# Optimization experiments

Measured on AMD Instinct MI355X. Metric: run time of the kernel, lower is better.

The kernel has to match this reference:

```python
import jax, jax.numpy as jnp
import numpy as np

B, S, D, H = 2, 2048, 2048, 16
HD = D // H  # head_dim = 128


def setup_inputs() -> dict:
    key = jax.random.key(0)
    k1, k2, k3, k4, k5, k6 = jax.random.split(key, 6)
    scale = 1.0 / np.sqrt(D)
    return {
        "hidden_states": jax.random.normal(k1, (B, S, D), dtype=jnp.float32),
        "attention_mask": jnp.ones((B, S), dtype=jnp.int32),
        "wq": jax.random.normal(k2, (D, D), dtype=jnp.float32) * scale,
        "wk": jax.random.normal(k3, (D, D), dtype=jnp.float32) * scale,
        "wv": jax.random.normal(k4, (D, D), dtype=jnp.float32) * scale,
        "wo": jax.random.normal(k5, (D, D), dtype=jnp.float32) * scale,
        "bo": jax.random.normal(k6, (D,), dtype=jnp.float32) * 0.01,
    }


def reference(hidden_states, attention_mask, wq, wk, wv, wo, bo):
    b, s, d = hidden_states.shape
    # QKV projections (no bias), split heads -> [B, S, H, HD]
    q = (hidden_states @ wq).reshape(b, s, H, HD)
    k = (hidden_states @ wk).reshape(b, s, H, HD)
    v = (hidden_states @ wv).reshape(b, s, H, HD)

    # combined causal + padding mask -> [B, 1, S, S]
    causal = jnp.tril(jnp.ones((s, s), dtype=bool))[None, None]
    pad = (attention_mask > 0)[:, None, None, :]  # [B,1,1,S]
    mask = jnp.logical_and(causal, pad)

    big_neg = jnp.finfo(hidden_states.dtype).min
    bias = jnp.where(mask, 0.0, big_neg).astype(hidden_states.dtype)

    # scaled dot-product attention (flax dot_product_attention scales by 1/sqrt(head_dim))
    scores = jnp.einsum("bqhd,bkhd->bhqk", q, k) / jnp.sqrt(jnp.asarray(HD, hidden_states.dtype))
    probs = jax.nn.softmax(scores + bias, axis=-1)
    ctx = jnp.einsum("bhqk,bkhd->bqhd", probs, v).reshape(b, s, d)

    return ctx @ wo + bo
```

## Files before the change

### kernel.cpp

```cpp
#include <hip/hip_runtime.h>
#include <hip/hip_bf16.h>
#include <stdint.h>

#define Bv 2
#define Sv 2048
#define Dv 2048
#define Hv 16
#define HDv 128
#define Mv (Bv*Sv)

typedef __attribute__((ext_vector_type(8))) short short8;
typedef __attribute__((ext_vector_type(4))) short short4v;
typedef __attribute__((ext_vector_type(4))) float f32x4;

__device__ __forceinline__ unsigned short bf16_rne(float f) {
    union { float f; uint32_t u; } c; c.f = f;
    uint32_t u = c.u;
    u += 0x7fffu + ((u >> 16) & 1u);
    return (unsigned short)(u >> 16);
}

__device__ __forceinline__ uint32_t cvt_pk_bf16(float lo, float hi) {
    uint32_t r;
    asm("v_cvt_pk_bf16_f32 %0, %1, %2" : "=v"(r) : "v"(lo), "v"(hi));
    return r;
}

__device__ __forceinline__ void gload16(const void* g, void* l) {
    __builtin_amdgcn_global_load_lds((const __attribute__((address_space(1))) void*)g,
                                     (__attribute__((address_space(3))) void*)l, 16, 0, 0);
}

#define BARRIER() asm volatile("s_barrier" ::: "memory")
#define LGKM0()   do { asm volatile("s_waitcnt lgkmcnt(0)" ::: "memory"); \
                       __builtin_amdgcn_sched_barrier(0); } while (0)

__global__ void cvt_x_kernel(const float* __restrict__ x, unsigned short* __restrict__ xb) {
    int i = (blockIdx.x * 256 + threadIdx.x) * 4;
    float4 v = *(const float4*)(x + i);
    short4v o;
    o[0] = (short)bf16_rne(v.x);
    o[1] = (short)bf16_rne(v.y);
    o[2] = (short)bf16_rne(v.z);
    o[3] = (short)bf16_rne(v.w);
    *(short4v*)(xb + i) = o;
}

__global__ void cvt_wt_kernel(const float* __restrict__ w0, const float* __restrict__ w1,
                              const float* __restrict__ w2, const float* __restrict__ w3,
                              unsigned short* __restrict__ wt) {
    __shared__ unsigned short t[64][65];
    int z = blockIdx.z;
    const float* w = (z == 0) ? w0 : (z == 1) ? w1 : (z == 2) ? w2 : w3;
    unsigned short* o = wt + (size_t)z * Dv * Dv;
    int k0 = blockIdx.x * 64, n0 = blockIdx.y * 64;
    for (int i = threadIdx.x; i < 4096; i += 256) {
        int r = i >> 6, c = i & 63;
        t[r][c] = bf16_rne(w[(size_t)(k0 + r) * Dv + n0 + c]);
    }
    __syncthreads();
    for (int i = threadIdx.x; i < 4096; i += 256) {
        int r = i >> 6, c = i & 63;
        o[(size_t)(n0 + r) * Dv + k0 + c] = t[c][r];
    }
}

__global__ void vt_kernel(const unsigned short* __restrict__ V, unsigned short* __restrict__ VT) {
    __shared__ unsigned short t[64 * 64];
    const int tid = threadIdx.x;
    const int b = blockIdx.z;
    const int s0 = blockIdx.x * 64, c0 = blockIdx.y * 64;
    const unsigned short* Vb = V + (size_t)b * Sv * Dv;
    unsigned short* VTb = VT + (size_t)b * Dv * Sv;
    #pragma unroll
    for (int ii = 0; ii < 2; ++ii) {
        int i = tid + ii * 256;
        int r = i >> 3, ch = i & 7;
        short8 v = *(const short8*)&Vb[(size_t)(s0 + r) * Dv + c0 + ch * 8];
        *(short8*)&t[r * 64 + ((ch ^ (r & 7)) << 3)] = v;
    }
    __syncthreads();
    #pragma unroll
    for (int ii = 0; ii < 2; ++ii) {
        int o = tid + ii * 256;
        int orow = o >> 3, och = o & 7;
        short8 v;
        #pragma unroll
        for (int j = 0; j < 8; ++j) {
            int r = och * 8 + j;
            int c = orow;
            v[j] = (short)t[r * 64 + ((((c >> 3) ^ (r & 7)) << 3) | (c & 7))];
        }
        *(short8*)&VTb[(size_t)(c0 + orow) * Sv + s0 + och * 8] = v;
    }
}

__global__ __launch_bounds__(512, 2) void gemm8ph_kernel(
    const unsigned short* __restrict__ A,
    const unsigned short* __restrict__ WtBase,
    unsigned short* __restrict__ CbBase)
{
    extern __shared__ unsigned short lds[];
    const int tid = threadIdx.x;
    const int wv = tid >> 6, ln = tid & 63;
    const int lr = ln & 15, lg = ln >> 4;
    const int wm = wv >> 2, wn = wv & 3;

    const int bid = blockIdx.x;
    const int xcd = bid & 7, idx = bid >> 3;
    const int n_idx = xcd * 2 + idx / 16;
    const int m_idx = idx % 16;
    const int m0 = m_idx * 256, n0g = n_idx * 256;

    const int lrow = wv * 8 + (ln >> 3);
    const int lcol = ((ln & 7) ^ (ln >> 3)) << 3;
    const unsigned short* Ag = A      + (size_t)(m0  + lrow) * Dv + lcol;
    const unsigned short* Bg = WtBase + (size_t)(n0g + lrow) * Dv + lcol;

    auto SH = [&](int T, int isB, int h) {
        const unsigned short* src = (isB ? Bg : Ag) + (size_t)(h * 128) * Dv + T * 64;
        unsigned short* dst = &lds[(T & 1) * 32768 + isB * 16384 + h * 8192 + wv * 512];
        gload16(src, dst);
        gload16(src + (size_t)64 * Dv, dst + 4096);
    };

    const int axk = lr & 7;
    auto RDA = [&](int buf, int fm, int ks) {
        return *(const short8*)&lds[buf * 32768 + (wm * 128 + fm * 16 + lr) * 64 + (((ks * 4 + lg) ^ axk) << 3)];
    };
    auto RDB = [&](int buf, int fn, int ks) {
        return *(const short8*)&lds[buf * 32768 + 16384 + (wn * 64 + fn * 16 + lr) * 64 + (((ks * 4 + lg) ^ axk) << 3)];
    };

    f32x4 acc[8][4];
    #pragma unroll
    for (int fm = 0; fm < 8; fm++)
        #pragma unroll
        for (int fn = 0; fn < 4; fn++)
            acc[fm][fn] = (f32x4){0.f, 0.f, 0.f, 0.f};

    SH(0, 0, 0); SH(0, 0, 1); SH(0, 1, 0); SH(0, 1, 1);
    SH(1, 1, 0); SH(1, 0, 0);
    asm volatile("s_waitcnt vmcnt(4)" ::: "memory");
    BARRIER();

    short8 af[8], b0[4], b1[4];
    const int NT2 = 16;

    #define MFMA_BLK(FN0, FN1, BARR) do {                                              \
        __builtin_amdgcn_s_setprio(1);                                                 \
        _Pragma("unroll")                                                              \
        for (int fm = 0; fm < 8; fm++) {                                               \
            acc[fm][FN0] = __builtin_amdgcn_mfma_f32_16x16x32_bf16(af[fm], BARR[FN0], acc[fm][FN0], 0, 0, 0); \
            acc[fm][FN1] = __builtin_amdgcn_mfma_f32_16x16x32_bf16(af[fm], BARR[FN1], acc[fm][FN1], 0, 0, 0); \
        }                                                                              \
        __builtin_amdgcn_s_setprio(0);                                                 \
    } while (0)

    for (int i = 0; i < NT2; ++i) {
        const int Tb = 2 * i + 1;
        const bool more = (i + 1 < NT2);

        #pragma unroll
        for (int fm = 0; fm < 8; fm++) af[fm] = RDA(0, fm, 0);
        #pragma unroll
        for (int fn = 0; fn < 4; fn++) b0[fn] = RDB(0, fn, 0);
        SH(Tb, 0, 1);
        BARRIER(); LGKM0();
        MFMA_BLK(0, 1, b0);
        BARRIER();

        #pragma unroll
        for (int fn = 0; fn < 4; fn++) b1[fn] = RDB(0, fn, 1);
        SH(Tb, 1, 1);
        BARRIER(); LGKM0();
        MFMA_BLK(2, 3, b0);
        BARRIER();

        #pragma unroll
        for (int fm = 0; fm < 8; fm++) af[fm] = RDA(0, fm, 1);
        if (more) SH(Tb + 1, 1, 0);
        BARRIER(); LGKM0();
        MFMA_BLK(0, 1, b1);
        BARRIER();

        if (more) SH(Tb + 1, 0, 0);
        BARRIER(); LGKM0();
        MFMA_BLK(2, 3, b1);
        if (more) asm volatile("s_waitcnt vmcnt(4)" ::: "memory");
        else      asm volatile("s_waitcnt vmcnt(0)" ::: "memory");
        BARRIER();

        #pragma unroll
        for (int fm = 0; fm < 8; fm++) af[fm] = RDA(1, fm, 0);
        #pragma unroll
        for (int fn = 0; fn < 4; fn++) b0[fn] = RDB(1, fn, 0);
        if (more) SH(Tb + 1, 0, 1);
        BARRIER(); LGKM0();
        MFMA_BLK(0, 1, b0);
        BARRIER();

        #pragma unroll
        for (int fn = 0; fn < 4; fn++) b1[fn] = RDB(1, fn, 1);
        if (more) SH(Tb + 1, 1, 1);
        BARRIER(); LGKM0();
        MFMA_BLK(2, 3, b0);
        BARRIER();

        #pragma unroll
        for (int fm = 0; fm < 8; fm++) af[fm] = RDA(1, fm, 1);
        if (more) SH(Tb + 2, 1, 0);
        BARRIER(); LGKM0();
        MFMA_BLK(0, 1, b1);
        BARRIER();

        if (more) SH(Tb + 2, 0, 0);
        BARRIER(); LGKM0();
        MFMA_BLK(2, 3, b1);
        if (more) {
            asm volatile("s_waitcnt vmcnt(4)" ::: "memory");
            BARRIER();
        }
    }
    #undef MFMA_BLK

    const int z = n0g >> 11;
    unsigned short* Cz = CbBase + (size_t)z * Mv * Dv;
    const int ncl = (n0g & 2047) + wn * 64;
    #pragma unroll
    for (int fm = 0; fm < 8; fm++)
        #pragma unroll
        for (int fn = 0; fn < 4; fn++) {
            int row = m0 + wm * 128 + fm * 16 + lg * 4;
            int col = ncl + fn * 16 + lr;
            #pragma unroll
            for (int r = 0; r < 4; r++)
                Cz[(size_t)(row + r) * Dv + col] = bf16_rne(acc[fm][fn][r]);
        }
}

template<int FOUT>
__global__ __launch_bounds__(512, 2) void gemm8_kernel(
    const unsigned short* __restrict__ A,
    const unsigned short* __restrict__ WtBase,
    unsigned short* __restrict__ Cb,
    float* __restrict__ Cf,
    const float* __restrict__ bias)
{
    extern __shared__ unsigned short lds[];
    const int tid = threadIdx.x;
    const int wv = tid >> 6, ln = tid & 63;
    const int lr = ln & 15, lg = ln >> 4;
    const int wm = wv >> 2, wn = wv & 3;

    const int bid = blockIdx.x;
    const int xcd = bid & 7, idx = bid >> 3;
    const int n_idx = xcd;
    const int m_idx = idx;
    const int m0 = m_idx * 128;
    const int n0g = n_idx * 256;
    const int NT = Dv / 64;

    const int srow = ln >> 3;
    const int swz = ((ln & 7) ^ srow) << 3;
    const unsigned short* Ab = A      + (size_t)(m0  + wv * 8 + srow) * Dv + swz;
    const unsigned short* Bb = WtBase + (size_t)(n0g + wv * 8 + srow) * Dv + swz;

    auto STAGE_A = [&](int t, int d) {
        const unsigned short* g = Ab + t * 64;
        #pragma unroll
        for (int j = 0; j < 2; ++j)
            gload16(g + (size_t)(j * 64) * Dv, &lds[d * 24576 + (j * 64 + wv * 8) * 64]);
    };
    auto STAGE_B = [&](int t, int d) {
        const unsigned short* g = Bb + t * 64;
        #pragma unroll
        for (int j = 0; j < 4; ++j)
            gload16(g + (size_t)(j * 64) * Dv, &lds[d * 24576 + 8192 + (j * 64 + wv * 8) * 64]);
    };

    const int aro = (wm * 64 + lr) * 64;
    const int bro = (wn * 64 + lr) * 64;
    const int ach0 = ((lg ^ (lr & 7)) << 3);
    const int ach1 = (((4 + lg) ^ (lr & 7)) << 3);

    f32x4 acc[4][4];
    #pragma unroll
    for (int mi = 0; mi < 4; mi++)
        #pragma unroll
        for (int ni = 0; ni < 4; ni++)
            acc[mi][ni] = (f32x4){0.f, 0.f, 0.f, 0.f};

    STAGE_A(0, 0); STAGE_B(0, 0);
    STAGE_A(1, 1); STAGE_B(1, 1);
    asm volatile("s_waitcnt vmcnt(6)" ::: "memory");
    BARRIER();

    for (int t = 0; t < NT; ++t) {
        const int d = t % 3, d2 = (t + 2) % 3;
        const unsigned short* la = &lds[d * 24576];
        const unsigned short* lb = &lds[d * 24576 + 8192];

        short8 af[4][2], bf0[2][2];
        #pragma unroll
        for (int mi = 0; mi < 4; mi++) {
            af[mi][0] = *(const short8*)&la[aro + mi * 1024 + ach0];
            af[mi][1] = *(const short8*)&la[aro + mi * 1024 + ach1];
        }
        #pragma unroll
        for (int ni = 0; ni < 2; ni++) {
            bf0[ni][0] = *(const short8*)&lb[bro + ni * 1024 + ach0];
            bf0[ni][1] = *(const short8*)&lb[bro + ni * 1024 + ach1];
        }
        if (t + 2 < NT) STAGE_A(t + 2, d2);
        BARRIER();
        __builtin_amdgcn_s_setprio(1);
        #pragma unroll
        for (int mi = 0; mi < 4; mi++)
            #pragma unroll
            for (int ni = 0; ni < 2; ni++) {
                acc[mi][ni] = __builtin_amdgcn_mfma_f32_16x16x32_bf16(af[mi][0], bf0[ni][0], acc[mi][ni], 0, 0, 0);
                acc[mi][ni] = __builtin_amdgcn_mfma_f32_16x16x32_bf16(af[mi][1], bf0[ni][1], acc[mi][ni], 0, 0, 0);
            }
        __builtin_amdgcn_s_setprio(0);

        short8 bf1[2][2];
        #pragma unroll
        for (int ni = 0; ni < 2; ni++) {
            bf1[ni][0] = *(const short8*)&lb[bro + (ni + 2) * 1024 + ach0];
            bf1[ni][1] = *(const short8*)&lb[bro + (ni + 2) * 1024 + ach1];
        }
        if (t + 2 < NT) STAGE_B(t + 2, d2);
        asm volatile("s_waitcnt vmcnt(6)" ::: "memory");
        BARRIER();
        __builtin_amdgcn_s_setprio(1);
        #pragma unroll
        for (int mi = 0; mi < 4; mi++)
            #pragma unroll
            for (int ni = 0; ni < 2; ni++) {
                acc[mi][ni + 2] = __builtin_amdgcn_mfma_f32_16x16x32_bf16(af[mi][0], bf1[ni][0], acc[mi][ni + 2], 0, 0, 0);
                acc[mi][ni + 2] = __builtin_amdgcn_mfma_f32_16x16x32_bf16(af[mi][1], bf1[ni][1], acc[mi][ni + 2], 0, 0, 0);
            }
        __builtin_amdgcn_s_setprio(0);
    }

    #pragma unroll
    for (int mi = 0; mi < 4; mi++)
        #pragma unroll
        for (int ni = 0; ni < 4; ni++) {
            int row = m0 + wm * 64 + mi * 16 + lg * 4;
            int col = n0g + wn * 64 + ni * 16 + lr;
            if (FOUT) {
                float bv = bias[col];
                #pragma unroll
                for (int r = 0; r < 4; r++)
                    Cf[(size_t)(row + r) * Dv + col] = acc[mi][ni][r] + bv;
            } else {
                #pragma unroll
                for (int r = 0; r < 4; r++)
                    Cb[(size_t)(row + r) * Dv + col] = bf16_rne(acc[mi][ni][r]);
            }
        }
}

__global__ __launch_bounds__(512) void attn_kernel(
    const unsigned short* __restrict__ Q, const unsigned short* __restrict__ K,
    const unsigned short* __restrict__ VT, const int* __restrict__ pmask,
    unsigned short* __restrict__ CTX)
{
    __shared__ unsigned short lK[2][64 * 128];
    __shared__ unsigned short lVt[2][128 * 64];
    __shared__ int lPmB[2][64];
    __shared__ int lPmOk[2];

    const int tid = threadIdx.x, wv = tid >> 6, ln = tid & 63;
    const int lr = ln & 15, lg = ln >> 4;
    const int L = blockIdx.x;
    const int bh = (L & 7) * 4 + ((L >> 3) & 3);
    const int b = bh >> 4, h = bh & 15;
    const int v = L >> 5;
    const int qidx = (v < 8) ? (15 - v) : (v - 8);
    const int q0 = qidx * 128;
    const int qw0 = q0 + wv * 16;
    const size_t hoff  = (size_t)b * Sv * Dv + (size_t)h * HDv;
    const size_t vtoff = ((size_t)b * Dv + (size_t)h * HDv) * Sv;

    short8 qf[4];
    #pragma unroll
    for (int ds = 0; ds < 4; ds++)
        qf[ds] = *(const short8*)&Q[hoff + (size_t)(qw0 + lr) * Dv + ds * 32 + lg * 8];

    size_t koff[2], voff[2];
    #pragma unroll
    for (int ii = 0; ii < 2; ++ii) {
        int slot = ii * 512 + wv * 64 + ln;
        int krow = slot >> 4, kch = slot & 15;
        koff[ii] = hoff + (size_t)krow * Dv + ((kch ^ (krow & 7)) << 3);
        int vrow = slot >> 3, vch = slot & 7;
        voff[ii] = vtoff + (size_t)vrow * Sv + ((vch ^ (vrow & 7)) << 3);
    }

    auto STAGE = [&](int t, int buf) {
        const size_t kadd = (size_t)(t << 6) * Dv;
        const int vadd = t << 6;
        unsigned short* kb = &lK[buf][0];
        unsigned short* vb = &lVt[buf][0];
        #pragma unroll
        for (int ii = 0; ii < 2; ++ii) {
            gload16(K + koff[ii] + kadd, kb + (ii * 512 + wv * 64) * 8);
            gload16(VT + voff[ii] + vadd, vb + (ii * 512 + wv * 64) * 8);
        }
        if (wv == 0) {
            int pmv = pmask[b * Sv + (t << 6) + ln];
            lPmB[buf][ln] = pmv;
            unsigned long long bal = __ballot(pmv != 0);
            if (ln == 0) lPmOk[buf] = (bal == ~0ull) ? 1 : 0;
        }
    };

    f32x4 acc[8];
    #pragma unroll
    for (int n = 0; n < 8; n++) acc[n] = (f32x4){0.f, 0.f, 0.f, 0.f};
    float mrow = -3.0e38f, lrow = 0.f;
    const float CS = 0.12751744f;
    const int qg = qw0 + lr;
    const int nt = (q0 >> 6) + 2;
    const int srcA = lr + ((lg & 1) << 5);
    const int srcB = srcA + 16;
    const bool hiSel = (lg >= 2);

    auto TILE = [&](int t, int buf, auto CAUSAL_c) {
        constexpr bool CAUSAL = decltype(CAUSAL_c)::value;
        const int kv0 = t << 6;
        const unsigned short* kb = &lK[buf][0];
        const unsigned short* vb = &lVt[buf][0];

        f32x4 st[4];
        #pragma unroll
        for (int t2 = 0; t2 < 4; ++t2) st[t2] = (f32x4){0.f, 0.f, 0.f, 0.f};
        __builtin_amdgcn_s_setprio(1);
        #pragma unroll
        for (int t2 = 0; t2 < 4; ++t2) {
            const int krow = t2 * 16 + lr;
            #pragma unroll
            for (int ds = 0; ds < 4; ++ds) {
                const int ch = ds * 4 + lg;
                short8 kf = *(const short8*)&kb[krow * 128 + ((ch ^ (krow & 7)) << 3)];
                st[t2] = __builtin_amdgcn_mfma_f32_16x16x32_bf16(kf, qf[ds], st[t2], 0, 0, 0);
            }
        }
        __builtin_amdgcn_s_setprio(0);

        float sv[4][4];
        float rmax;
        if constexpr (CAUSAL) {
            const int* pm = &lPmB[buf][0];
            #pragma unroll
            for (int t2 = 0; t2 < 4; ++t2)
                #pragma unroll
                for (int r = 0; r < 4; ++r) {
                    int kvl = t2 * 16 + lg * 4 + r;
                    bool ok = ((kv0 + kvl) <= qg) && (pm[kvl] != 0);
                    sv[t2][r] = ok ? st[t2][r] * CS : -1.0e30f;
                }
            rmax = sv[0][0];
            #pragma unroll
            for (int t2 = 0; t2 < 4; ++t2)
                #pragma unroll
                for (int r = 0; r < 4; ++r) rmax = fmaxf(rmax, sv[t2][r]);
            rmax = fmaxf(rmax, __shfl_xor(rmax, 16, 64));
            rmax = fmaxf(rmax, __shfl_xor(rmax, 32, 64));
        } else {
            rmax = st[0][0];
            #pragma unroll
            for (int t2 = 0; t2 < 4; ++t2)
                #pragma unroll
                for (int r = 0; r < 4; ++r) rmax = fmaxf(rmax, st[t2][r]);
            rmax = fmaxf(rmax, __shfl_xor(rmax, 16, 64));
            rmax = fmaxf(rmax, __shfl_xor(rmax, 32, 64));
            rmax *= CS;
        }

        if (!__all(rmax - mrow <= 8.0f)) {
            float mn = fmaxf(mrow, rmax);
            float alpha = exp2f(mrow - mn);
            mrow = mn;
            lrow *= alpha;
            #pragma unroll
            for (int n = 0; n < 8; n++)
                #pragma unroll
                for (int r = 0; r < 4; r++) acc[n][r] *= alpha;
        }

        float p[4][4]; float psum = 0.f;
        if constexpr (CAUSAL) {
            #pragma unroll
            for (int t2 = 0; t2 < 4; ++t2)
                #pragma unroll
                for (int r = 0; r < 4; ++r) {
                    float e = exp2f(sv[t2][r] - mrow);
                    p[t2][r] = (sv[t2][r] > -5.0e29f) ? e : 0.f;
                    psum += p[t2][r];
                }
        } else {
            if (lPmOk[buf]) {
                #pragma unroll
                for (int t2 = 0; t2 < 4; ++t2)
                    #pragma unroll
                    for (int r = 0; r < 4; ++r) {
                        p[t2][r] = exp2f(fmaf(st[t2][r], CS, -mrow));
                        psum += p[t2][r];
                    }
            } else {
                const int* pm = &lPmB[buf][0];
                #pragma unroll
                for (int t2 = 0; t2 < 4; ++t2)
                    #pragma unroll
                    for (int r = 0; r < 4; ++r) {
                        int kvl = t2 * 16 + lg * 4 + r;
                        float e = exp2f(fmaf(st[t2][r], CS, -mrow));
                        p[t2][r] = (pm[kvl] != 0) ? e : 0.f;
                        psum += p[t2][r];
                    }
            }
        }
        psum += __shfl_xor(psum, 16, 64);
        psum += __shfl_xor(psum, 32, 64);
        lrow += psum;

        uint32_t pk[4][2];
        #pragma unroll
        for (int t2 = 0; t2 < 4; ++t2)
            #pragma unroll
            for (int pp = 0; pp < 2; ++pp)
                pk[t2][pp] = cvt_pk_bf16(p[t2][2 * pp], p[t2][2 * pp + 1]);

        union U { uint32_t u[4]; short8 s; } pa0, pa1;
        {
            uint32_t l0 = (uint32_t)__shfl((int)pk[0][0], srcA, 64), h0 = (uint32_t)__shfl((int)pk[1][0], srcA, 64);
            uint32_t l1 = (uint32_t)__shfl((int)pk[0][1], srcA, 64), h1 = (uint32_t)__shfl((int)pk[1][1], srcA, 64);
            uint32_t l2 = (uint32_t)__shfl((int)pk[0][0], srcB, 64), h2 = (uint32_t)__shfl((int)pk[1][0], srcB, 64);
            uint32_t l3 = (uint32_t)__shfl((int)pk[0][1], srcB, 64), h3 = (uint32_t)__shfl((int)pk[1][1], srcB, 64);
            pa0.u[0] = hiSel ? h0 : l0; pa0.u[1] = hiSel ? h1 : l1;
            pa0.u[2] = hiSel ? h2 : l2; pa0.u[3] = hiSel ? h3 : l3;
        }
        {
            uint32_t l0 = (uint32_t)__shfl((int)pk[2][0], srcA, 64), h0 = (uint32_t)__shfl((int)pk[3][0], srcA, 64);
            uint32_t l1 = (uint32_t)__shfl((int)pk[2][1], srcA, 64), h1 = (uint32_t)__shfl((int)pk[3][1], srcA, 64);
            uint32_t l2 = (uint32_t)__shfl((int)pk[2][0], srcB, 64), h2 = (uint32_t)__shfl((int)pk[3][0], srcB, 64);
            uint32_t l3 = (uint32_t)__shfl((int)pk[2][1], srcB, 64), h3 = (uint32_t)__shfl((int)pk[3][1], srcB, 64);
            pa1.u[0] = hiSel ? h0 : l0; pa1.u[1] = hiSel ? h1 : l1;
            pa1.u[2] = hiSel ? h2 : l2; pa1.u[3] = hiSel ? h3 : l3;
        }

        __builtin_amdgcn_s_setprio(1);
        #pragma unroll
        for (int n = 0; n < 8; n++) {
            const int vrow = n * 16 + lr;
            short8 a0 = *(const short8*)&vb[vrow * 64 + ((lg ^ (vrow & 7)) << 3)];
            acc[n] = __builtin_amdgcn_mfma_f32_16x16x32_bf16(a0, pa0.s, acc[n], 0, 0, 0);
            short8 a1 = *(const short8*)&vb[vrow * 64 + (((4 + lg) ^ (vrow & 7)) << 3)];
            acc[n] = __builtin_amdgcn_mfma_f32_16x16x32_bf16(a1, pa1.s, acc[n], 0, 0, 0);
        }
        __builtin_amdgcn_s_setprio(0);
    };

    STAGE(0, 0);
    __syncthreads();
    int cur = 0;

    for (int t = 0; t < nt; ++t) {
        if (t + 1 < nt) STAGE(t + 1, cur ^ 1);
        const int kv0 = t << 6;
        if (kv0 <= qw0 + 15) {
            if (kv0 + 63 > qw0) TILE(t, cur, std::integral_constant<bool, true>{});
            else                TILE(t, cur, std::integral_constant<bool, false>{});
        }
        __syncthreads();
        cur ^= 1;
    }

    float inv = 1.0f / lrow;
    #pragma unroll
    for (int n = 0; n < 8; n++) {
        short4v o;
        #pragma unroll
        for (int r = 0; r < 4; r++) o[r] = (short)bf16_rne(acc[n][r] * inv);
        *(short4v*)&CTX[hoff + (size_t)qg * Dv + n * 16 + lg * 4] = o;
    }
}

extern "C" void kernel_launch(void* const* d_in, const int* in_sizes, int n_in,
                              void* d_out, int out_size, void* d_ws, size_t ws_size,
                              hipStream_t stream) {
    const float* hs  = (const float*)d_in[0];
    const int*   am  = (const int*)d_in[1];
    const float* wq  = (const float*)d_in[2];
    const float* wk  = (const float*)d_in[3];
    const float* wv_ = (const float*)d_in[4];
    const float* wo  = (const float*)d_in[5];
    const float* bo  = (const float*)d_in[6];
    float* out = (float*)d_out;

    char* ws = (char*)d_ws;
    unsigned short* Xb  = (unsigned short*)ws;
    unsigned short* Wt  = (unsigned short*)(ws + (size_t)16 * 1024 * 1024);
    unsigned short* QKV = (unsigned short*)(ws + (size_t)48 * 1024 * 1024);
    unsigned short* CTX = (unsigned short*)(ws + (size_t)96 * 1024 * 1024);
    unsigned short* VT  = Xb;

    const int LDSB_8PH = 131072;
    const int LDSB_R   = 147456;
    static bool attrSet = false;
    if (!attrSet) {
        hipFuncSetAttribute((const void*)gemm8ph_kernel, hipFuncAttributeMaxDynamicSharedMemorySize, LDSB_8PH);
        hipFuncSetAttribute((const void*)gemm8_kernel<0>, hipFuncAttributeMaxDynamicSharedMemorySize, LDSB_R);
        hipFuncSetAttribute((const void*)gemm8_kernel<1>, hipFuncAttributeMaxDynamicSharedMemorySize, LDSB_R);
        attrSet = true;
    }

    hipLaunchKernelGGL(cvt_x_kernel, dim3(Mv * Dv / 4 / 256), dim3(256), 0, stream, hs, Xb);
    hipLaunchKernelGGL(cvt_wt_kernel, dim3(32, 32, 4), dim3(256), 0, stream, wq, wk, wv_, wo, Wt);
    hipLaunchKernelGGL(gemm8ph_kernel, dim3(256), dim3(512), LDSB_8PH, stream, Xb, Wt, QKV);
    hipLaunchKernelGGL(gemm8_kernel<0>, dim3(256), dim3(512), LDSB_R, stream,
                       Xb, Wt + 2 * (size_t)Dv * Dv, QKV + 2 * (size_t)Mv * Dv, (float*)nullptr, (const float*)nullptr);
    hipLaunchKernelGGL(vt_kernel, dim3(32, 32, 2), dim3(256), 0, stream,
                       QKV + 2 * (size_t)Mv * Dv, VT);
    hipLaunchKernelGGL(attn_kernel, dim3(512), dim3(512), 0, stream,
                       QKV, QKV + (size_t)Mv * Dv, VT, am, CTX);
    hipLaunchKernelGGL(gemm8_kernel<1>, dim3(256), dim3(512), LDSB_R, stream,
                       CTX, Wt + 3 * (size_t)Dv * Dv, (unsigned short*)nullptr, out, bo);
}
```

Baseline: 237.7 us.

## Pair low and high causal query tiles per block to share K/V tiles

Each attention block now handles two 128-row query tiles, a low one and its mirror high one, with separate accumulators and softmax state. Each staged K/V tile feeds both groups, so LDS K/V fragments are reused and the causal work per block is balanced. The grid drops from 512 to 256 blocks. The cost is roughly doubled accumulator registers, which may lower occupancy, plus fewer blocks to spread across the CUs.

```diff
diff --git a/kernel.cpp b/kernel.cpp
--- a/kernel.cpp
+++ b/kernel.cpp
@@ -12,6 +12,8 @@
 typedef __attribute__((ext_vector_type(8))) short short8;
 typedef __attribute__((ext_vector_type(4))) short short4v;
 typedef __attribute__((ext_vector_type(4))) float f32x4;
+
+union PU { uint32_t u[4]; short8 s; };
 
 __device__ __forceinline__ unsigned short bf16_rne(float f) {
     union { float f; uint32_t u; } c; c.f = f;
@@ -378,17 +380,18 @@
     const int L = blockIdx.x;
     const int bh = (L & 7) * 4 + ((L >> 3) & 3);
     const int b = bh >> 4, h = bh & 15;
-    const int v = L >> 5;
-    const int qidx = (v < 8) ? (15 - v) : (v - 8);
-    const int q0 = qidx * 128;
-    const int qw0 = q0 + wv * 16;
+    const int p = L >> 5;
+    const int q0l = p * 128, q0h = (15 - p) * 128;
+    const int qw0l = q0l + wv * 16, qw0h = q0h + wv * 16;
     const size_t hoff  = (size_t)b * Sv * Dv + (size_t)h * HDv;
     const size_t vtoff = ((size_t)b * Dv + (size_t)h * HDv) * Sv;
 
-    short8 qf[4];
-    #pragma unroll
-    for (int ds = 0; ds < 4; ds++)
-        qf[ds] = *(const short8*)&Q[hoff + (size_t)(qw0 + lr) * Dv + ds * 32 + lg * 8];
+    short8 qfL[4], qfH[4];
+    #pragma unroll
+    for (int ds = 0; ds < 4; ds++) {
+        qfL[ds] = *(const short8*)&Q[hoff + (size_t)(qw0l + lr) * Dv + ds * 32 + lg * 8];
+        qfH[ds] = *(const short8*)&Q[hoff + (size_t)(qw0h + lr) * Dv + ds * 32 + lg * 8];
+    }
 
     size_t koff[2], voff[2];
     #pragma unroll
@@ -418,42 +421,27 @@
         }
     };
 
-    f32x4 acc[8];
-    #pragma unroll
-    for (int n = 0; n < 8; n++) acc[n] = (f32x4){0.f, 0.f, 0.f, 0.f};
-    float mrow = -3.0e38f, lrow = 0.f;
+    f32x4 accL[8], accH[8];
+    #pragma unroll
+    for (int n = 0; n < 8; n++) {
+        accL[n] = (f32x4){0.f, 0.f, 0.f, 0.f};
+        accH[n] = (f32x4){0.f, 0.f, 0.f, 0.f};
+    }
+    float mrowL = -3.0e38f, lrowL = 0.f;
+    float mrowH = -3.0e38f, lrowH = 0.f;
     const float CS = 0.12751744f;
-    const int qg = qw0 + lr;
-    const int nt = (q0 >> 6) + 2;
+    const int qgL = qw0l + lr, qgH = qw0h + lr;
+    const int nt = (q0h >> 6) + 2;
     const int srcA = lr + ((lg & 1) << 5);
     const int srcB = srcA + 16;
     const bool hiSel = (lg >= 2);
 
-    auto TILE = [&](int t, int buf, auto CAUSAL_c) {
-        constexpr bool CAUSAL = decltype(CAUSAL_c)::value;
-        const int kv0 = t << 6;
-        const unsigned short* kb = &lK[buf][0];
-        const unsigned short* vb = &lVt[buf][0];
-
-        f32x4 st[4];
-        #pragma unroll
-        for (int t2 = 0; t2 < 4; ++t2) st[t2] = (f32x4){0.f, 0.f, 0.f, 0.f};
-        __builtin_amdgcn_s_setprio(1);
-        #pragma unroll
-        for (int t2 = 0; t2 < 4; ++t2) {
-            const int krow = t2 * 16 + lr;
-            #pragma unroll
-            for (int ds = 0; ds < 4; ++ds) {
-                const int ch = ds * 4 + lg;
-                short8 kf = *(const short8*)&kb[krow * 128 + ((ch ^ (krow & 7)) << 3)];
-                st[t2] = __builtin_amdgcn_mfma_f32_16x16x32_bf16(kf, qf[ds], st[t2], 0, 0, 0);
-            }
-        }
-        __builtin_amdgcn_s_setprio(0);
-
+    auto GROUP_SM = [&](const f32x4 (&st)[4], f32x4 (&acc)[8], float& mrow, float& lrow,
+                        int qg, int kv0, int buf, PU& pa0, PU& pa1, auto DIAG_c) {
+        constexpr bool DIAG = decltype(DIAG_c)::value;
         float sv[4][4];
         float rmax;
-        if constexpr (CAUSAL) {
+        if constexpr (DIAG) {
             const int* pm = &lPmB[buf][0];
             #pragma unroll
             for (int t2 = 0; t2 < 4; ++t2)
@@ -492,15 +480,15 @@
                 for (int r = 0; r < 4; r++) acc[n][r] *= alpha;
         }
 
-        float p[4][4]; float psum = 0.f;
-        if constexpr (CAUSAL) {
+        float pr[4][4]; float psum = 0.f;
+        if constexpr (DIAG) {
             #pragma unroll
             for (int t2 = 0; t2 < 4; ++t2)
                 #pragma unroll
                 for (int r = 0; r < 4; ++r) {
                     float e = exp2f(sv[t2][r] - mrow);
-                    p[t2][r] = (sv[t2][r] > -5.0e29f) ? e : 0.f;
-                    psum += p[t2][r];
+                    pr[t2][r] = (sv[t2][r] > -5.0e29f) ? e : 0.f;
+                    psum += pr[t2][r];
                 }
         } else {
             if (lPmOk[buf]) {
@@ -508,8 +496,8 @@
                 for (int t2 = 0; t2 < 4; ++t2)
                     #pragma unroll
                     for (int r = 0; r < 4; ++r) {
-                        p[t2][r] = exp2f(fmaf(st[t2][r], CS, -mrow));
-                        psum += p[t2][r];
+                        pr[t2][r] = exp2f(fmaf(st[t2][r], CS, -mrow));
+                        psum += pr[t2][r];
                     }
             } else {
                 const int* pm = &lPmB[buf][0];
@@ -519,8 +507,8 @@
                     for (int r = 0; r < 4; ++r) {
                         int kvl = t2 * 16 + lg * 4 + r;
                         float e = exp2f(fmaf(st[t2][r], CS, -mrow));
-                        p[t2][r] = (pm[kvl] != 0) ? e : 0.f;
-                        psum += p[t2][r];
+                        pr[t2][r] = (pm[kvl] != 0) ? e : 0.f;
+                        psum += pr[t2][r];
                     }
             }
         }
@@ -533,9 +521,8 @@
         for (int t2 = 0; t2 < 4; ++t2)
             #pragma unroll
             for (int pp = 0; pp < 2; ++pp)
-                pk[t2][pp] = cvt_pk_bf16(p[t2][2 * pp], p[t2][2 * pp + 1]);
-
-        union U { uint32_t u[4]; short8 s; } pa0, pa1;
+                pk[t2][pp] = cvt_pk_bf16(pr[t2][2 * pp], pr[t2][2 * pp + 1]);
+
         {
             uint32_t l0 = (uint32_t)__shfl((int)pk[0][0], srcA, 64), h0 = (uint32_t)__shfl((int)pk[1][0], srcA, 64);
             uint32_t l1 = (uint32_t)__shfl((int)pk[0][1], srcA, 64), h1 = (uint32_t)__shfl((int)pk[1][1], srcA, 64);
@@ -552,15 +539,52 @@
             pa1.u[0] = hiSel ? h0 : l0; pa1.u[1] = hiSel ? h1 : l1;
             pa1.u[2] = hiSel ? h2 : l2; pa1.u[3] = hiSel ? h3 : l3;
         }
+    };
+
+    auto TILE = [&](int t, int buf, auto DOL_c, auto DIAG_c) {
+        constexpr bool DOL = decltype(DOL_c)::value;
+        const int kv0 = t << 6;
+        const unsigned short* kb = &lK[buf][0];
+        const unsigned short* vb = &lVt[buf][0];
+
+        f32x4 stL[4], stH[4];
+        #pragma unroll
+        for (int t2 = 0; t2 < 4; ++t2) {
+            stH[t2] = (f32x4){0.f, 0.f, 0.f, 0.f};
+            if constexpr (DOL) stL[t2] = (f32x4){0.f, 0.f, 0.f, 0.f};
+        }
+        __builtin_amdgcn_s_setprio(1);
+        #pragma unroll
+        for (int t2 = 0; t2 < 4; ++t2) {
+            const int krow = t2 * 16 + lr;
+            #pragma unroll
+            for (int ds = 0; ds < 4; ++ds) {
+                const int ch = ds * 4 + lg;
+                short8 kf = *(const short8*)&kb[krow * 128 + ((ch ^ (krow & 7)) << 3)];
+                stH[t2] = __builtin_amdgcn_mfma_f32_16x16x32_bf16(kf, qfH[ds], stH[t2], 0, 0, 0);
+                if constexpr (DOL)
+                    stL[t2] = __builtin_amdgcn_mfma_f32_16x16x32_bf16(kf, qfL[ds], stL[t2], 0, 0, 0);
+            }
+        }
+        __builtin_amdgcn_s_setprio(0);
+
+        PU paH0, paH1, paL0, paL1;
+        GROUP_SM(stH, accH, mrowH, lrowH, qgH, kv0, buf, paH0, paH1, DIAG_c);
+        if constexpr (DOL)
+            GROUP_SM(stL, accL, mrowL, lrowL, qgL, kv0, buf, paL0, paL1, DIAG_c);
 
         __builtin_amdgcn_s_setprio(1);
         #pragma unroll
         for (int n = 0; n < 8; n++) {
             const int vrow = n * 16 + lr;
             short8 a0 = *(const short8*)&vb[vrow * 64 + ((lg ^ (vrow & 7)) << 3)];
-            acc[n] = __builtin_amdgcn_mfma_f32_16x16x32_bf16(a0, pa0.s, acc[n], 0, 0, 0);
             short8 a1 = *(const short8*)&vb[vrow * 64 + (((4 + lg) ^ (vrow & 7)) << 3)];
-            acc[n] = __builtin_amdgcn_mfma_f32_16x16x32_bf16(a1, pa1.s, acc[n], 0, 0, 0);
+            accH[n] = __builtin_amdgcn_mfma_f32_16x16x32_bf16(a0, paH0.s, accH[n], 0, 0, 0);
+            accH[n] = __builtin_amdgcn_mfma_f32_16x16x32_bf16(a1, paH1.s, accH[n], 0, 0, 0);
+            if constexpr (DOL) {
+                accL[n] = __builtin_amdgcn_mfma_f32_16x16x32_bf16(a0, paL0.s, accL[n], 0, 0, 0);
+                accL[n] = __builtin_amdgcn_mfma_f32_16x16x32_bf16(a1, paL1.s, accL[n], 0, 0, 0);
+            }
         }
         __builtin_amdgcn_s_setprio(0);
     };
@@ -569,24 +593,38 @@
     __syncthreads();
     int cur = 0;
 
+    using TrueC  = std::integral_constant<bool, true>;
+    using FalseC = std::integral_constant<bool, false>;
+
     for (int t = 0; t < nt; ++t) {
         if (t + 1 < nt) STAGE(t + 1, cur ^ 1);
         const int kv0 = t << 6;
-        if (kv0 <= qw0 + 15) {
-            if (kv0 + 63 > qw0) TILE(t, cur, std::integral_constant<bool, true>{});
-            else                TILE(t, cur, std::integral_constant<bool, false>{});
+        if (kv0 <= qw0h + 15) {
+            const bool doL = (kv0 <= qw0l + 15);
+            const bool diag = (kv0 + 63 > qw0h) || (doL && (kv0 + 63 > qw0l));
+            if (doL) {
+                if (diag) TILE(t, cur, TrueC{}, TrueC{});
+                else      TILE(t, cur, TrueC{}, FalseC{});
+            } else {
+                if (diag) TILE(t, cur, FalseC{}, TrueC{});
+                else      TILE(t, cur, FalseC{}, FalseC{});
+            }
         }
         __syncthreads();
         cur ^= 1;
     }
 
-    float inv = 1.0f / lrow;
+    float invL = 1.0f / lrowL, invH = 1.0f / lrowH;
     #pragma unroll
     for (int n = 0; n < 8; n++) {
-        short4v o;
-        #pragma unroll
-        for (int r = 0; r < 4; r++) o[r] = (short)bf16_rne(acc[n][r] * inv);
-        *(short4v*)&CTX[hoff + (size_t)qg * Dv + n * 16 + lg * 4] = o;
+        short4v oL, oH;
+        #pragma unroll
+        for (int r = 0; r < 4; r++) {
+            oL[r] = (short)bf16_rne(accL[n][r] * invL);
+            oH[r] = (short)bf16_rne(accH[n][r] * invH);
+        }
+        *(short4v*)&CTX[hoff + (size_t)qgL * Dv + n * 16 + lg * 4] = oL;
+        *(short4v*)&CTX[hoff + (size_t)qgH * Dv + n * 16 + lg * 4] = oH;
     }
 }
 
@@ -626,7 +664,7 @@
                        Xb, Wt + 2 * (size_t)Dv * Dv, QKV + 2 * (size_t)Mv * Dv, (float*)nullptr, (const float*)nullptr);
     hipLaunchKernelGGL(vt_kernel, dim3(32, 32, 2), dim3(256), 0, stream,
                        QKV + 2 * (size_t)Mv * Dv, VT);
-    hipLaunchKernelGGL(attn_kernel, dim3(512), dim3(512), 0, stream,
+    hipLaunchKernelGGL(attn_kernel, dim3(256), dim3(512), 0, stream,
                        QKV, QKV + (size_t)Mv * Dv, VT, am, CTX);
     hipLaunchKernelGGL(gemm8_kernel<1>, dim3(256), dim3(512), LDSB_R, stream,
                        CTX, Wt + 3 * (size_t)Dv * Dv, (unsigned short*)nullptr, out, bo);
```

Measured after the change: 242.0 us. No clear change (+1.8%).

## Switch attention to 32x32x16 MFMA with 4 waves of 32 query rows

Applied to the files above, without the earlier changes.

The attention kernel moves from 16x16x32 MFMA tiles with 8 waves of 16 query rows each to 32x32x16 MFMA tiles with 4 waves of 32 query rows each. Blocks shrink to 256 threads, and each thread stages 4 K/V chunks instead of 2. The P-to-operand reshuffle becomes a single lane^32 swap, and the row reductions need fewer cross-lane shuffles. The aim is better MFMA throughput and less LDS re-reading of K/V per query row. In exchange, per-wave register pressure rises and the causal skip becomes coarser at 32-row granularity.

```diff
diff --git a/kernel.cpp b/kernel.cpp
--- a/kernel.cpp
+++ b/kernel.cpp
@@ -12,6 +12,9 @@
 typedef __attribute__((ext_vector_type(8))) short short8;
 typedef __attribute__((ext_vector_type(4))) short short4v;
 typedef __attribute__((ext_vector_type(4))) float f32x4;
+typedef __attribute__((ext_vector_type(16))) float f32x16;
+
+union PU { uint32_t u[4]; short8 s; };
 
 __device__ __forceinline__ unsigned short bf16_rne(float f) {
     union { float f; uint32_t u; } c; c.f = f;
@@ -363,7 +366,7 @@
         }
 }
 
-__global__ __launch_bounds__(512) void attn_kernel(
+__global__ __launch_bounds__(256) void attn_kernel(
     const unsigned short* __restrict__ Q, const unsigned short* __restrict__ K,
     const unsigned short* __restrict__ VT, const int* __restrict__ pmask,
     unsigned short* __restrict__ CTX)
@@ -374,26 +377,27 @@
     __shared__ int lPmOk[2];
 
     const int tid = threadIdx.x, wv = tid >> 6, ln = tid & 63;
-    const int lr = ln & 15, lg = ln >> 4;
+    const int lq = ln & 31, lh = ln >> 5;
     const int L = blockIdx.x;
     const int bh = (L & 7) * 4 + ((L >> 3) & 3);
     const int b = bh >> 4, h = bh & 15;
     const int v = L >> 5;
     const int qidx = (v < 8) ? (15 - v) : (v - 8);
     const int q0 = qidx * 128;
-    const int qw0 = q0 + wv * 16;
+    const int qw0 = q0 + wv * 32;
+    const int qg = qw0 + lq;
     const size_t hoff  = (size_t)b * Sv * Dv + (size_t)h * HDv;
     const size_t vtoff = ((size_t)b * Dv + (size_t)h * HDv) * Sv;
 
-    short8 qf[4];
-    #pragma unroll
-    for (int ds = 0; ds < 4; ds++)
-        qf[ds] = *(const short8*)&Q[hoff + (size_t)(qw0 + lr) * Dv + ds * 32 + lg * 8];
-
-    size_t koff[2], voff[2];
-    #pragma unroll
-    for (int ii = 0; ii < 2; ++ii) {
-        int slot = ii * 512 + wv * 64 + ln;
+    short8 qf[8];
+    #pragma unroll
+    for (int ds = 0; ds < 8; ds++)
+        qf[ds] = *(const short8*)&Q[hoff + (size_t)qg * Dv + ds * 16 + lh * 8];
+
+    size_t koff[4], voff[4];
+    #pragma unroll
+    for (int ii = 0; ii < 4; ++ii) {
+        int slot = ii * 256 + tid;
         int krow = slot >> 4, kch = slot & 15;
         koff[ii] = hoff + (size_t)krow * Dv + ((kch ^ (krow & 7)) << 3);
         int vrow = slot >> 3, vch = slot & 7;
@@ -406,9 +410,9 @@
         unsigned short* kb = &lK[buf][0];
         unsigned short* vb = &lVt[buf][0];
         #pragma unroll
-        for (int ii = 0; ii < 2; ++ii) {
-            gload16(K + koff[ii] + kadd, kb + (ii * 512 + wv * 64) * 8);
-            gload16(VT + voff[ii] + vadd, vb + (ii * 512 + wv * 64) * 8);
+        for (int ii = 0; ii < 4; ++ii) {
+            gload16(K + koff[ii] + kadd, kb + (ii * 256 + wv * 64) * 8);
+            gload16(VT + voff[ii] + vadd, vb + (ii * 256 + wv * 64) * 8);
         }
         if (wv == 0) {
             int pmv = pmask[b * Sv + (t << 6) + ln];
@@ -418,65 +422,67 @@
         }
     };
 
-    f32x4 acc[8];
-    #pragma unroll
-    for (int n = 0; n < 8; n++) acc[n] = (f32x4){0.f, 0.f, 0.f, 0.f};
+    f32x16 acc[4];
+    #pragma unroll
+    for (int db = 0; db < 4; db++)
+        #pragma unroll
+        for (int e = 0; e < 16; e++) acc[db][e] = 0.f;
+
     float mrow = -3.0e38f, lrow = 0.f;
     const float CS = 0.12751744f;
-    const int qg = qw0 + lr;
     const int nt = (q0 >> 6) + 2;
-    const int srcA = lr + ((lg & 1) << 5);
-    const int srcB = srcA + 16;
-    const bool hiSel = (lg >= 2);
-
-    auto TILE = [&](int t, int buf, auto CAUSAL_c) {
-        constexpr bool CAUSAL = decltype(CAUSAL_c)::value;
+    const int pl = ln ^ 32;
+    const bool hi = (lh == 1);
+
+    auto TILE = [&](int t, int buf, auto DIAG_c) {
+        constexpr bool DIAG = decltype(DIAG_c)::value;
         const int kv0 = t << 6;
         const unsigned short* kb = &lK[buf][0];
         const unsigned short* vb = &lVt[buf][0];
 
-        f32x4 st[4];
-        #pragma unroll
-        for (int t2 = 0; t2 < 4; ++t2) st[t2] = (f32x4){0.f, 0.f, 0.f, 0.f};
+        f32x16 st[2];
+        #pragma unroll
+        for (int kvb = 0; kvb < 2; ++kvb)
+            #pragma unroll
+            for (int e = 0; e < 16; e++) st[kvb][e] = 0.f;
+
         __builtin_amdgcn_s_setprio(1);
         #pragma unroll
-        for (int t2 = 0; t2 < 4; ++t2) {
-            const int krow = t2 * 16 + lr;
-            #pragma unroll
-            for (int ds = 0; ds < 4; ++ds) {
-                const int ch = ds * 4 + lg;
-                short8 kf = *(const short8*)&kb[krow * 128 + ((ch ^ (krow & 7)) << 3)];
-                st[t2] = __builtin_amdgcn_mfma_f32_16x16x32_bf16(kf, qf[ds], st[t2], 0, 0, 0);
+        for (int kvb = 0; kvb < 2; ++kvb) {
+            const int krow = kvb * 32 + lq;
+            const int r7 = krow & 7;
+            #pragma unroll
+            for (int ds = 0; ds < 8; ++ds) {
+                short8 kf = *(const short8*)&kb[krow * 128 + (((ds * 2 + lh) ^ r7) << 3)];
+                st[kvb] = __builtin_amdgcn_mfma_f32_32x32x16_bf16(kf, qf[ds], st[kvb], 0, 0, 0);
             }
         }
         __builtin_amdgcn_s_setprio(0);
 
-        float sv[4][4];
+        float pv[2][16];
         float rmax;
-        if constexpr (CAUSAL) {
+        if constexpr (DIAG) {
             const int* pm = &lPmB[buf][0];
             #pragma unroll
-            for (int t2 = 0; t2 < 4; ++t2)
-                #pragma unroll
-                for (int r = 0; r < 4; ++r) {
-                    int kvl = t2 * 16 + lg * 4 + r;
+            for (int kvb = 0; kvb < 2; ++kvb)
+                #pragma unroll
+                for (int e = 0; e < 16; ++e) {
+                    int kvl = kvb * 32 + (e & 3) + 8 * (e >> 2) + 4 * lh;
                     bool ok = ((kv0 + kvl) <= qg) && (pm[kvl] != 0);
-                    sv[t2][r] = ok ? st[t2][r] * CS : -1.0e30f;
+                    pv[kvb][e] = ok ? st[kvb][e] * CS : -1.0e30f;
                 }
-            rmax = sv[0][0];
-            #pragma unroll
-            for (int t2 = 0; t2 < 4; ++t2)
-                #pragma unroll
-                for (int r = 0; r < 4; ++r) rmax = fmaxf(rmax, sv[t2][r]);
-            rmax = fmaxf(rmax, __shfl_xor(rmax, 16, 64));
+            rmax = pv[0][0];
+            #pragma unroll
+            for (int kvb = 0; kvb < 2; ++kvb)
+                #pragma unroll
+                for (int e = 0; e < 16; ++e) rmax = fmaxf(rmax, pv[kvb][e]);
             rmax = fmaxf(rmax, __shfl_xor(rmax, 32, 64));
         } else {
             rmax = st[0][0];
             #pragma unroll
-            for (int t2 = 0; t2 < 4; ++t2)
-                #pragma unroll
-                for (int r = 0; r < 4; ++r) rmax = fmaxf(rmax, st[t2][r]);
-            rmax = fmaxf(rmax, __shfl_xor(rmax, 16, 64));
+            for (int kvb = 0; kvb < 2; ++kvb)
+                #pragma unroll
+                for (int e = 0; e < 16; ++e) rmax = fmaxf(rmax, st[kvb][e]);
             rmax = fmaxf(rmax, __shfl_xor(rmax, 32, 64));
             rmax *= CS;
         }
@@ -487,80 +493,79 @@
             mrow = mn;
             lrow *= alpha;
             #pragma unroll
-            for (int n = 0; n < 8; n++)
-                #pragma unroll
-                for (int r = 0; r < 4; r++) acc[n][r] *= alpha;
-        }
-
-        float p[4][4]; float psum = 0.f;
-        if constexpr (CAUSAL) {
-            #pragma unroll
-            for (int t2 = 0; t2 < 4; ++t2)
-                #pragma unroll
-                for (int r = 0; r < 4; ++r) {
-                    float e = exp2f(sv[t2][r] - mrow);
-                    p[t2][r] = (sv[t2][r] > -5.0e29f) ? e : 0.f;
-                    psum += p[t2][r];
+            for (int db = 0; db < 4; db++) acc[db] *= alpha;
+        }
+
+        float psum = 0.f;
+        if constexpr (DIAG) {
+            #pragma unroll
+            for (int kvb = 0; kvb < 2; ++kvb)
+                #pragma unroll
+                for (int e = 0; e < 16; ++e) {
+                    float ex = exp2f(pv[kvb][e] - mrow);
+                    pv[kvb][e] = (pv[kvb][e] > -5.0e29f) ? ex : 0.f;
+                    psum += pv[kvb][e];
                 }
         } else {
             if (lPmOk[buf]) {
                 #pragma unroll
-                for (int t2 = 0; t2 < 4; ++t2)
+                for (int kvb = 0; kvb < 2; ++kvb)
                     #pragma unroll
-                    for (int r = 0; r < 4; ++r) {
-                        p[t2][r] = exp2f(fmaf(st[t2][r], CS, -mrow));
-                        psum += p[t2][r];
+                    for (int e = 0; e < 16; ++e) {
+                        pv[kvb][e] = exp2f(fmaf(st[kvb][e], CS, -mrow));
+                        psum += pv[kvb][e];
                     }
             } else {
                 const int* pm = &lPmB[buf][0];
                 #pragma unroll
-                for (int t2 = 0; t2 < 4; ++t2)
+                for (int kvb = 0; kvb < 2; ++kvb)
                     #pragma unroll
-                    for (int r = 0; r < 4; ++r) {
-                        int kvl = t2 * 16 + lg * 4 + r;
-                        float e = exp2f(fmaf(st[t2][r], CS, -mrow));
-                        p[t2][r] = (pm[kvl] != 0) ? e : 0.f;
-                        psum += p[t2][r];
+                    for (int e = 0; e < 16; ++e) {
+                        int kvl = kvb * 32 + (e & 3) + 8 * (e >> 2) + 4 * lh;
+                        float ex = exp2f(fmaf(st[kvb][e], CS, -mrow));
+                        pv[kvb][e] = (pm[kvl] != 0) ? ex : 0.f;
+                        psum += pv[kvb][e];
                     }
             }
         }
-        psum += __shfl_xor(psum, 16, 64);
         psum += __shfl_xor(psum, 32, 64);
         lrow += psum;
 
-        uint32_t pk[4][2];
-        #pragma unroll
-        for (int t2 = 0; t2 < 4; ++t2)
-            #pragma unroll
-            for (int pp = 0; pp < 2; ++pp)
-                pk[t2][pp] = cvt_pk_bf16(p[t2][2 * pp], p[t2][2 * pp + 1]);
-
-        union U { uint32_t u[4]; short8 s; } pa0, pa1;
-        {
-            uint32_t l0 = (uint32_t)__shfl((int)pk[0][0], srcA, 64), h0 = (uint32_t)__shfl((int)pk[1][0], srcA, 64);
-            uint32_t l1 = (uint32_t)__shfl((int)pk[0][1], srcA, 64), h1 = (uint32_t)__shfl((int)pk[1][1], srcA, 64);
-            uint32_t l2 = (uint32_t)__shfl((int)pk[0][0], srcB, 64), h2 = (uint32_t)__shfl((int)pk[1][0], srcB, 64);
-            uint32_t l3 = (uint32_t)__shfl((int)pk[0][1], srcB, 64), h3 = (uint32_t)__shfl((int)pk[1][1], srcB, 64);
-            pa0.u[0] = hiSel ? h0 : l0; pa0.u[1] = hiSel ? h1 : l1;
-            pa0.u[2] = hiSel ? h2 : l2; pa0.u[3] = hiSel ? h3 : l3;
-        }
-        {
-            uint32_t l0 = (uint32_t)__shfl((int)pk[2][0], srcA, 64), h0 = (uint32_t)__shfl((int)pk[3][0], srcA, 64);
-            uint32_t l1 = (uint32_t)__shfl((int)pk[2][1], srcA, 64), h1 = (uint32_t)__shfl((int)pk[3][1], srcA, 64);
-            uint32_t l2 = (uint32_t)__shfl((int)pk[2][0], srcB, 64), h2 = (uint32_t)__shfl((int)pk[3][0], srcB, 64);
-            uint32_t l3 = (uint32_t)__shfl((int)pk[2][1], srcB, 64), h3 = (uint32_t)__shfl((int)pk[3][1], srcB, 64);
-            pa1.u[0] = hiSel ? h0 : l0; pa1.u[1] = hiSel ? h1 : l1;
-            pa1.u[2] = hiSel ? h2 : l2; pa1.u[3] = hiSel ? h3 : l3;
+        PU pf[4];
+        #pragma unroll
+        for (int kvb = 0; kvb < 2; ++kvb) {
+            uint32_t a0 = cvt_pk_bf16(pv[kvb][0],  pv[kvb][1]);
+            uint32_t a1 = cvt_pk_bf16(pv[kvb][2],  pv[kvb][3]);
+            uint32_t b0 = cvt_pk_bf16(pv[kvb][4],  pv[kvb][5]);
+            uint32_t b1 = cvt_pk_bf16(pv[kvb][6],  pv[kvb][7]);
+            uint32_t c0 = cvt_pk_bf16(pv[kvb][8],  pv[kvb][9]);
+            uint32_t c1 = cvt_pk_bf16(pv[kvb][10], pv[kvb][11]);
+            uint32_t d0 = cvt_pk_bf16(pv[kvb][12], pv[kvb][13]);
+            uint32_t d1 = cvt_pk_bf16(pv[kvb][14], pv[kvb][15]);
+            uint32_t pa0 = (uint32_t)__shfl((int)a0, pl, 64), pa1 = (uint32_t)__shfl((int)a1, pl, 64);
+            uint32_t pb0 = (uint32_t)__shfl((int)b0, pl, 64), pb1 = (uint32_t)__shfl((int)b1, pl, 64);
+            uint32_t pc0 = (uint32_t)__shfl((int)c0, pl, 64), pc1 = (uint32_t)__shfl((int)c1, pl, 64);
+            uint32_t pd0 = (uint32_t)__shfl((int)d0, pl, 64), pd1 = (uint32_t)__shfl((int)d1, pl, 64);
+            pf[kvb * 2 + 0].u[0] = hi ? pb0 : a0;
+            pf[kvb * 2 + 0].u[1] = hi ? pb1 : a1;
+            pf[kvb * 2 + 0].u[2] = hi ? b0 : pa0;
+            pf[kvb * 2 + 0].u[3] = hi ? b1 : pa1;
+            pf[kvb * 2 + 1].u[0] = hi ? pd0 : c0;
+            pf[kvb * 2 + 1].u[1] = hi ? pd1 : c1;
+            pf[kvb * 2 + 1].u[2] = hi ? d0 : pc0;
+            pf[kvb * 2 + 1].u[3] = hi ? d1 : pc1;
         }
 
         __builtin_amdgcn_s_setprio(1);
         #pragma unroll
-        for (int n = 0; n < 8; n++) {
-            const int vrow = n * 16 + lr;
-            short8 a0 = *(const short8*)&vb[vrow * 64 + ((lg ^ (vrow & 7)) << 3)];
-            acc[n] = __builtin_amdgcn_mfma_f32_16x16x32_bf16(a0, pa0.s, acc[n], 0, 0, 0);
-            short8 a1 = *(const short8*)&vb[vrow * 64 + (((4 + lg) ^ (vrow & 7)) << 3)];
-            acc[n] = __builtin_amdgcn_mfma_f32_16x16x32_bf16(a1, pa1.s, acc[n], 0, 0, 0);
+        for (int db = 0; db < 4; ++db) {
+            const int vrow = db * 32 + lq;
+            const int r7 = vrow & 7;
+            #pragma unroll
+            for (int kb = 0; kb < 4; ++kb) {
+                short8 vf = *(const short8*)&vb[vrow * 64 + (((kb * 2 + lh) ^ r7) << 3)];
+                acc[db] = __builtin_amdgcn_mfma_f32_32x32x16_bf16(vf, pf[kb].s, acc[db], 0, 0, 0);
+            }
         }
         __builtin_amdgcn_s_setprio(0);
     };
@@ -569,12 +574,15 @@
     __syncthreads();
     int cur = 0;
 
+    using TrueC  = std::integral_constant<bool, true>;
+    using FalseC = std::integral_constant<bool, false>;
+
     for (int t = 0; t < nt; ++t) {
         if (t + 1 < nt) STAGE(t + 1, cur ^ 1);
         const int kv0 = t << 6;
-        if (kv0 <= qw0 + 15) {
-            if (kv0 + 63 > qw0) TILE(t, cur, std::integral_constant<bool, true>{});
-            else                TILE(t, cur, std::integral_constant<bool, false>{});
+        if (kv0 <= qw0 + 31) {
+            if (kv0 + 63 > qw0) TILE(t, cur, TrueC{});
+            else                TILE(t, cur, FalseC{});
         }
         __syncthreads();
         cur ^= 1;
@@ -582,12 +590,14 @@
 
     float inv = 1.0f / lrow;
     #pragma unroll
-    for (int n = 0; n < 8; n++) {
-        short4v o;
-        #pragma unroll
-        for (int r = 0; r < 4; r++) o[r] = (short)bf16_rne(acc[n][r] * inv);
-        *(short4v*)&CTX[hoff + (size_t)qg * Dv + n * 16 + lg * 4] = o;
-    }
+    for (int db = 0; db < 4; ++db)
+        #pragma unroll
+        for (int q2 = 0; q2 < 4; ++q2) {
+            short4v o;
+            #pragma unroll
+            for (int r = 0; r < 4; r++) o[r] = (short)bf16_rne(acc[db][q2 * 4 + r] * inv);
+            *(short4v*)&CTX[hoff + (size_t)qg * Dv + db * 32 + q2 * 8 + lh * 4] = o;
+        }
 }
 
 extern "C" void kernel_launch(void* const* d_in, const int* in_sizes, int n_in,
@@ -626,7 +636,7 @@
                        Xb, Wt + 2 * (size_t)Dv * Dv, QKV + 2 * (size_t)Mv * Dv, (float*)nullptr, (const float*)nullptr);
     hipLaunchKernelGGL(vt_kernel, dim3(32, 32, 2), dim3(256), 0, stream,
                        QKV + 2 * (size_t)Mv * Dv, VT);
-    hipLaunchKernelGGL(attn_kernel, dim3(512), dim3(512), 0, stream,
+    hipLaunchKernelGGL(attn_kernel, dim3(512), dim3(256), 0, stream,
                        QKV, QKV + (size_t)Mv * Dv, VT, am, CTX);
     hipLaunchKernelGGL(gemm8_kernel<1>, dim3(256), dim3(512), LDSB_R, stream,
                        CTX, Wt + 3 * (size_t)Dv * Dv, (unsigned short*)nullptr, out, bo);
```

After: 281.1 us. 1.18x slower.
